# Kernel optimization log

Hardware: AMD Instinct MI355X
Metric: run time of the kernel (lower is better)

Reference implementation:

```python
import jax, jax.numpy as jnp
import numpy as np

# ogbn-products-like 3-layer GraphSAGE mini-batch: fanouts [15, 10, 5], batch 1024
N0, N1, N2, N3 = 1_000_000, 67_584, 6_144, 1_024
F_IN, HID, OUT = 100, 256, 47
FAN1, FAN2, FAN3 = 15, 10, 5
E1, E2, E3 = N1 * FAN1, N2 * FAN2, N3 * FAN3


def _glorot(key, shape):
    lim = np.sqrt(6.0 / (shape[0] + shape[1])).astype(np.float32)
    return jax.random.uniform(key, shape, jnp.float32, -lim, lim)


def setup_inputs() -> dict:
    key = jax.random.key(0)
    ks = jax.random.split(key, 12)
    x = jax.random.normal(ks[0], (N0, F_IN), jnp.float32)
    # bipartite edge lists: src indexes into the layer's source nodes,
    # dst indexes into the first n_dst nodes (the targets)
    src1 = jax.random.randint(ks[1], (E1,), 0, N0, jnp.int64)
    dst1 = jnp.repeat(jnp.arange(N1, dtype=jnp.int64), FAN1)
    src2 = jax.random.randint(ks[2], (E2,), 0, N1, jnp.int64)
    dst2 = jnp.repeat(jnp.arange(N2, dtype=jnp.int64), FAN2)
    src3 = jax.random.randint(ks[3], (E3,), 0, N2, jnp.int64)
    dst3 = jnp.repeat(jnp.arange(N3, dtype=jnp.int64), FAN3)
    return {
        "x": x,
        "W_l1": _glorot(ks[4], (F_IN, HID)), "W_r1": _glorot(ks[5], (F_IN, HID)), "b1": jnp.zeros((HID,), jnp.float32),
        "W_l2": _glorot(ks[6], (HID, HID)), "W_r2": _glorot(ks[7], (HID, HID)), "b2": jnp.zeros((HID,), jnp.float32),
        "W_l3": _glorot(ks[8], (HID, OUT)), "W_r3": _glorot(ks[9], (HID, OUT)), "b3": jnp.zeros((OUT,), jnp.float32),
        "src1": src1, "dst1": dst1, "src2": src2, "dst2": dst2, "src3": src3, "dst3": dst3,
    }


def _sage_conv(x_src, x_dst, src, dst, W_l, W_r, b, n_dst):
    # mean aggregation over incoming edges, then out = lin_l(agg) + lin_r(x_dst)
    msg = x_src[src]                                             # [E, d]
    agg = jax.ops.segment_sum(msg, dst, num_segments=n_dst)      # [n_dst, d]
    cnt = jax.ops.segment_sum(jnp.ones((src.shape[0],), x_src.dtype), dst,
                              num_segments=n_dst)
    agg = agg / jnp.maximum(cnt, 1.0)[:, None]
    return agg @ W_l + x_dst @ W_r + b


def reference(x, W_l1, W_r1, b1, W_l2, W_r2, b2, W_l3, W_r3, b3,
              src1, dst1, src2, dst2, src3, dst3):
    h = _sage_conv(x, x[:N1], src1, dst1, W_l1, W_r1, b1, N1)
    h = jax.nn.relu(h)                                           # dropout in eval mode = identity
    h = _sage_conv(h, h[:N2], src2, dst2, W_l2, W_r2, b2, N2)
    h = jax.nn.relu(h)
    h = _sage_conv(h, h[:N3], src3, dst3, W_l3, W_r3, b3, N3)
    return jax.nn.log_softmax(h, axis=-1)                        # [N3, OUT]
```

## Files before the change

### kernel.cpp

```cpp
#include <hip/hip_runtime.h>
#include <math.h>

static constexpr int cN1 = 67584, cN2 = 6144, cN3 = 1024;
static constexpr int F_IN = 100, HID = 256, OUT = 47;
static constexpr int K1P = 224;

typedef __attribute__((ext_vector_type(8))) short short8;
typedef __attribute__((ext_vector_type(4))) float float4v;

__device__ __forceinline__ ushort f2b(float f) {
    unsigned u = __builtin_bit_cast(unsigned, f);
    u += 0x7fff + ((u >> 16) & 1);
    return (ushort)(u >> 16);
}
__device__ __forceinline__ float b2f(ushort h) {
    unsigned u = ((unsigned)h) << 16;
    return __builtin_bit_cast(float, u);
}

__global__ void build_A1(const float* __restrict__ x, const int* __restrict__ src,
                         ushort* __restrict__ A1)
{
    int wave = (int)((blockIdx.x * blockDim.x + threadIdx.x) >> 6);
    int lane = threadIdx.x & 63;
    if (wave >= cN1) return;
    const int* s = src + (size_t)wave * 15;
    float ax = 0.f, ay = 0.f;
    #pragma unroll
    for (int k = 0; k < 15; ++k) {
        const float2* row = (const float2*)(x + (size_t)s[k] * F_IN);
        if (lane < 50) { float2 v = row[lane]; ax += v.x; ay += v.y; }
    }
    ushort* out = A1 + (size_t)wave * K1P;
    if (lane < 50) {
        float2 o = ((const float2*)(x + (size_t)wave * F_IN))[lane];
        ushort2 m; m.x = f2b(ax * (1.0f / 15.0f)); m.y = f2b(ay * (1.0f / 15.0f));
        ((ushort2*)out)[lane] = m;
        ushort2 d; d.x = f2b(o.x); d.y = f2b(o.y);
        *(ushort2*)(out + 100 + 2 * lane) = d;
    } else if (lane < 62) {
        ushort2 z; z.x = 0; z.y = 0;
        *(ushort2*)(out + 200 + 2 * (lane - 50)) = z;
    }
}

template<int FAN>
__global__ void build_A(const ushort* __restrict__ H, const int* __restrict__ src,
                        ushort* __restrict__ A, int M)
{
    int wave = (int)((blockIdx.x * blockDim.x + threadIdx.x) >> 6);
    int lane = threadIdx.x & 63;
    if (wave >= M) return;
    const int* s = src + (size_t)wave * FAN;
    float a0 = 0.f, a1 = 0.f, a2 = 0.f, a3 = 0.f;
    #pragma unroll
    for (int k = 0; k < FAN; ++k) {
        ushort4 v = ((const ushort4*)(H + (size_t)s[k] * HID))[lane];
        a0 += b2f(v.x); a1 += b2f(v.y); a2 += b2f(v.z); a3 += b2f(v.w);
    }
    const float inv = 1.0f / (float)FAN;
    ushort4 own = ((const ushort4*)(H + (size_t)wave * HID))[lane];
    ushort* out = A + (size_t)wave * (2 * HID);
    ushort4 m; m.x = f2b(a0 * inv); m.y = f2b(a1 * inv); m.z = f2b(a2 * inv); m.w = f2b(a3 * inv);
    ((ushort4*)out)[lane] = m;
    ((ushort4*)(out + HID))[lane] = own;
}

__global__ void conv_W(const float* __restrict__ Wl, const float* __restrict__ Wr,
                       ushort* __restrict__ Bt, int K1, int N, int Npad, int Kpad)
{
    int idx = blockIdx.x * blockDim.x + threadIdx.x;
    if (idx >= Npad * Kpad) return;
    int n = idx / Kpad, k = idx - n * Kpad;
    float v = 0.f;
    if (n < N) {
        if (k < K1)           v = Wl[(size_t)k * N + n];
        else if (k < 2 * K1)  v = Wr[(size_t)(k - K1) * N + n];
    }
    Bt[idx] = f2b(v);
}

template<bool OUT_BF16, bool RELU>
__launch_bounds__(256)
__global__ void mfma_gemm(const ushort* __restrict__ A, const ushort* __restrict__ Bt,
                          const float* __restrict__ bias, void* __restrict__ Cout,
                          int M, int N, int K)
{
    constexpr int BM = 128, BK = 32, SA = BK + 8;
    __shared__ ushort As[BM * SA];
    __shared__ ushort Bs[BM * SA];
    const int tid  = threadIdx.x;
    const int m0   = blockIdx.y * BM;
    const int n0   = blockIdx.x * BM;
    const int lane = tid & 63;
    const int w    = tid >> 6;
    const int wr   = (w >> 1) * 64;
    const int wc   = (w & 1) * 64;
    const int m_in = lane & 15;
    const int k8   = (lane >> 4) * 8;
    const int srow = tid >> 1;
    const int skc  = (tid & 1) * 16;

    float4v acc[4][4] = {};

    const ushort* gA = A  + (size_t)(m0 + srow) * K + skc;
    const ushort* gB = Bt + (size_t)(n0 + srow) * K + skc;

    for (int k0 = 0; k0 < K; k0 += BK) {
        float4 a0 = ((const float4*)(gA + k0))[0];
        float4 a1 = ((const float4*)(gA + k0))[1];
        float4 b0 = ((const float4*)(gB + k0))[0];
        float4 b1 = ((const float4*)(gB + k0))[1];
        __syncthreads();
        *(float4*)&As[srow * SA + skc]     = a0;
        *(float4*)&As[srow * SA + skc + 8] = a1;
        *(float4*)&Bs[srow * SA + skc]     = b0;
        *(float4*)&Bs[srow * SA + skc + 8] = b1;
        __syncthreads();
        short8 af[4], bf[4];
        #pragma unroll
        for (int i = 0; i < 4; ++i) {
            af[i] = *(const short8*)&As[(wr + i * 16 + m_in) * SA + k8];
            bf[i] = *(const short8*)&Bs[(wc + i * 16 + m_in) * SA + k8];
        }
        #pragma unroll
        for (int mi = 0; mi < 4; ++mi)
            #pragma unroll
            for (int ni = 0; ni < 4; ++ni)
                acc[mi][ni] = __builtin_amdgcn_mfma_f32_16x16x32_bf16(af[mi], bf[ni], acc[mi][ni], 0, 0, 0);
    }

    #pragma unroll
    for (int ni = 0; ni < 4; ++ni) {
        int col = n0 + wc + ni * 16 + m_in;
        if (col >= N) continue;
        float bv = bias[col];
        #pragma unroll
        for (int mi = 0; mi < 4; ++mi) {
            #pragma unroll
            for (int r = 0; r < 4; ++r) {
                int row = m0 + wr + mi * 16 + (lane >> 4) * 4 + r;
                float v = acc[mi][ni][r] + bv;
                if (RELU) v = fmaxf(v, 0.f);
                if (OUT_BF16) ((ushort*)Cout)[(size_t)row * N + col] = f2b(v);
                else          ((float*)Cout)[(size_t)row * N + col] = v;
            }
        }
    }
}

__global__ void logsoftmax_kernel(float* __restrict__ out, int M, int N)
{
    int wave = (int)((blockIdx.x * blockDim.x + threadIdx.x) >> 6);
    int lane = threadIdx.x & 63;
    if (wave >= M) return;
    float* row = out + (size_t)wave * N;
    float v = (lane < N) ? row[lane] : -INFINITY;
    float m = v;
    #pragma unroll
    for (int off = 32; off; off >>= 1) m = fmaxf(m, __shfl_xor(m, off));
    float e = (lane < N) ? expf(v - m) : 0.f;
    float s = e;
    #pragma unroll
    for (int off = 32; off; off >>= 1) s += __shfl_xor(s, off);
    float ls = logf(s);
    if (lane < N) row[lane] = v - m - ls;
}

extern "C" void kernel_launch(void* const* d_in, const int* in_sizes, int n_in,
                              void* d_out, int out_size, void* d_ws, size_t ws_size,
                              hipStream_t stream)
{
    const float* x    = (const float*)d_in[0];
    const float* W_l1 = (const float*)d_in[1];
    const float* W_r1 = (const float*)d_in[2];
    const float* b1   = (const float*)d_in[3];
    const float* W_l2 = (const float*)d_in[4];
    const float* W_r2 = (const float*)d_in[5];
    const float* b2   = (const float*)d_in[6];
    const float* W_l3 = (const float*)d_in[7];
    const float* W_r3 = (const float*)d_in[8];
    const float* b3   = (const float*)d_in[9];
    const int* src1 = (const int*)d_in[10];
    const int* src2 = (const int*)d_in[12];
    const int* src3 = (const int*)d_in[14];
    float* out = (float*)d_out;

    ushort* ws  = (ushort*)d_ws;
    ushort* A1  = ws;
    ushort* h1  = A1  + (size_t)cN1 * K1P;
    ushort* A2  = h1  + (size_t)cN1 * HID;
    ushort* h2  = A2  + (size_t)cN2 * 2 * HID;
    ushort* A3  = h2  + (size_t)cN2 * HID;
    ushort* Bt1 = A3  + (size_t)cN3 * 2 * HID;
    ushort* Bt2 = Bt1 + (size_t)256 * K1P;
    ushort* Bt3 = Bt2 + (size_t)256 * 2 * HID;

    conv_W<<<(256 * K1P + 255) / 256, 256, 0, stream>>>(W_l1, W_r1, Bt1, F_IN, HID, 256, K1P);
    conv_W<<<(256 * 512 + 255) / 256, 256, 0, stream>>>(W_l2, W_r2, Bt2, HID, HID, 256, 512);
    conv_W<<<(128 * 512 + 255) / 256, 256, 0, stream>>>(W_l3, W_r3, Bt3, HID, OUT, 128, 512);

    build_A1<<<cN1 / 4, 256, 0, stream>>>(x, src1, A1);
    mfma_gemm<true, true><<<dim3(2, cN1 / 128), 256, 0, stream>>>(A1, Bt1, b1, h1, cN1, HID, K1P);
    build_A<10><<<cN2 / 4, 256, 0, stream>>>(h1, src2, A2, cN2);
    mfma_gemm<true, true><<<dim3(2, cN2 / 128), 256, 0, stream>>>(A2, Bt2, b2, h2, cN2, HID, 512);
    build_A<5><<<cN3 / 4, 256, 0, stream>>>(h2, src3, A3, cN3);
    mfma_gemm<false, false><<<dim3(1, cN3 / 128), 256, 0, stream>>>(A3, Bt3, b3, out, cN3, OUT, 512);
    logsoftmax_kernel<<<cN3 / 4, 256, 0, stream>>>(out, cN3, OUT);
}
```

Measured before the change: 687.0 us.

## Widen gather loads with half-wave edge split, fuse weight conversion and log-softmax

The gather kernels now split edges between the two half-waves, which load 16-byte vectors and combine their sums with a cross-half shuffle, replacing narrower per-lane loads. The three weight-conversion launches become a single kernel, and log-softmax moves into the epilogue of the final GEMM so the last output round-trip and one launch go away. This reduces the number of memory transactions in the latency-bound gathers and the launch count. The costs are extra shuffles and more complex epilogue code.

```diff
diff --git a/kernel.cpp b/kernel.cpp
--- a/kernel.cpp
+++ b/kernel.cpp
@@ -13,9 +13,8 @@
     u += 0x7fff + ((u >> 16) & 1);
     return (ushort)(u >> 16);
 }
-__device__ __forceinline__ float b2f(ushort h) {
-    unsigned u = ((unsigned)h) << 16;
-    return __builtin_bit_cast(float, u);
+__device__ __forceinline__ unsigned pack2(float a, float b) {
+    return (unsigned)f2b(a) | ((unsigned)f2b(b) << 16);
 }
 
 __global__ void build_A1(const float* __restrict__ x, const int* __restrict__ src,
@@ -25,22 +24,40 @@
     int lane = threadIdx.x & 63;
     if (wave >= cN1) return;
     const int* s = src + (size_t)wave * 15;
-    float ax = 0.f, ay = 0.f;
-    #pragma unroll
-    for (int k = 0; k < 15; ++k) {
-        const float2* row = (const float2*)(x + (size_t)s[k] * F_IN);
-        if (lane < 50) { float2 v = row[lane]; ax += v.x; ay += v.y; }
-    }
-    ushort* out = A1 + (size_t)wave * K1P;
-    if (lane < 50) {
-        float2 o = ((const float2*)(x + (size_t)wave * F_IN))[lane];
-        ushort2 m; m.x = f2b(ax * (1.0f / 15.0f)); m.y = f2b(ay * (1.0f / 15.0f));
-        ((ushort2*)out)[lane] = m;
-        ushort2 d; d.x = f2b(o.x); d.y = f2b(o.y);
-        *(ushort2*)(out + 100 + 2 * lane) = d;
-    } else if (lane < 62) {
-        ushort2 z; z.x = 0; z.y = 0;
-        *(ushort2*)(out + 200 + 2 * (lane - 50)) = z;
+    const int half = lane >> 5, hl = lane & 31;
+    const bool act = hl < 25;
+    float4 own = {0.f, 0.f, 0.f, 0.f};
+    if (half == 1 && act)
+        own = *(const float4*)(x + (size_t)wave * F_IN + 4 * hl);
+    float4 acc = {0.f, 0.f, 0.f, 0.f};
+    #pragma unroll
+    for (int j = 0; j < 8; ++j) {
+        int e = 2 * j + half;
+        if (e < 15 && act) {
+            float4 v = *(const float4*)(x + (size_t)s[e] * F_IN + 4 * hl);
+            acc.x += v.x; acc.y += v.y; acc.z += v.z; acc.w += v.w;
+        }
+    }
+    acc.x += __shfl(acc.x, lane ^ 32);
+    acc.y += __shfl(acc.y, lane ^ 32);
+    acc.z += __shfl(acc.z, lane ^ 32);
+    acc.w += __shfl(acc.w, lane ^ 32);
+    ushort* outp = A1 + (size_t)wave * K1P;
+    constexpr float inv = 1.0f / 15.0f;
+    if (half == 0) {
+        if (act) {
+            ushort4 m; m.x = f2b(acc.x * inv); m.y = f2b(acc.y * inv);
+                       m.z = f2b(acc.z * inv); m.w = f2b(acc.w * inv);
+            *(ushort4*)(outp + 4 * hl) = m;
+        }
+    } else {
+        if (act) {
+            ushort4 d; d.x = f2b(own.x); d.y = f2b(own.y); d.z = f2b(own.z); d.w = f2b(own.w);
+            *(ushort4*)(outp + 100 + 4 * hl) = d;
+        } else if (hl < 31) {
+            ushort4 z; z.x = 0; z.y = 0; z.z = 0; z.w = 0;
+            *(ushort4*)(outp + 200 + 4 * (hl - 25)) = z;
+        }
     }
 }
 
@@ -52,35 +69,74 @@
     int lane = threadIdx.x & 63;
     if (wave >= M) return;
     const int* s = src + (size_t)wave * FAN;
-    float a0 = 0.f, a1 = 0.f, a2 = 0.f, a3 = 0.f;
-    #pragma unroll
-    for (int k = 0; k < FAN; ++k) {
-        ushort4 v = ((const ushort4*)(H + (size_t)s[k] * HID))[lane];
-        a0 += b2f(v.x); a1 += b2f(v.y); a2 += b2f(v.z); a3 += b2f(v.w);
-    }
-    const float inv = 1.0f / (float)FAN;
-    ushort4 own = ((const ushort4*)(H + (size_t)wave * HID))[lane];
-    ushort* out = A + (size_t)wave * (2 * HID);
-    ushort4 m; m.x = f2b(a0 * inv); m.y = f2b(a1 * inv); m.z = f2b(a2 * inv); m.w = f2b(a3 * inv);
-    ((ushort4*)out)[lane] = m;
-    ((ushort4*)(out + HID))[lane] = own;
-}
-
-__global__ void conv_W(const float* __restrict__ Wl, const float* __restrict__ Wr,
-                       ushort* __restrict__ Bt, int K1, int N, int Npad, int Kpad)
-{
-    int idx = blockIdx.x * blockDim.x + threadIdx.x;
-    if (idx >= Npad * Kpad) return;
-    int n = idx / Kpad, k = idx - n * Kpad;
-    float v = 0.f;
-    if (n < N) {
-        if (k < K1)           v = Wl[(size_t)k * N + n];
-        else if (k < 2 * K1)  v = Wr[(size_t)(k - K1) * N + n];
-    }
-    Bt[idx] = f2b(v);
-}
-
-template<bool OUT_BF16, bool RELU>
+    const int half = lane >> 5, hl = lane & 31;
+    const float* Hf = (const float*)H;
+    float4 own;
+    if (half == 1)
+        own = *(const float4*)(Hf + (size_t)wave * 128 + 4 * hl);
+    float a[8] = {0.f, 0.f, 0.f, 0.f, 0.f, 0.f, 0.f, 0.f};
+    constexpr int NJ = (FAN + 1) / 2;
+    #pragma unroll
+    for (int j = 0; j < NJ; ++j) {
+        int e = 2 * j + half;
+        if (e < FAN) {
+            float4 v = *(const float4*)(Hf + (size_t)s[e] * 128 + 4 * hl);
+            unsigned u;
+            u = __builtin_bit_cast(unsigned, v.x);
+            a[0] += __builtin_bit_cast(float, u << 16); a[1] += __builtin_bit_cast(float, u & 0xffff0000u);
+            u = __builtin_bit_cast(unsigned, v.y);
+            a[2] += __builtin_bit_cast(float, u << 16); a[3] += __builtin_bit_cast(float, u & 0xffff0000u);
+            u = __builtin_bit_cast(unsigned, v.z);
+            a[4] += __builtin_bit_cast(float, u << 16); a[5] += __builtin_bit_cast(float, u & 0xffff0000u);
+            u = __builtin_bit_cast(unsigned, v.w);
+            a[6] += __builtin_bit_cast(float, u << 16); a[7] += __builtin_bit_cast(float, u & 0xffff0000u);
+        }
+    }
+    #pragma unroll
+    for (int i = 0; i < 8; ++i) a[i] += __shfl(a[i], lane ^ 32);
+    ushort* outp = A + (size_t)wave * (2 * HID);
+    constexpr float inv = 1.0f / (float)FAN;
+    if (half == 0) {
+        uint4 w;
+        w.x = pack2(a[0] * inv, a[1] * inv);
+        w.y = pack2(a[2] * inv, a[3] * inv);
+        w.z = pack2(a[4] * inv, a[5] * inv);
+        w.w = pack2(a[6] * inv, a[7] * inv);
+        *(uint4*)(outp + 8 * hl) = w;
+    } else {
+        *(float4*)(outp + HID + 8 * hl) = own;
+    }
+}
+
+static constexpr int S1 = 256 * K1P, S2 = 256 * 512, S3 = 128 * 512;
+__global__ void conv_W_all(const float* __restrict__ Wl1, const float* __restrict__ Wr1,
+                           const float* __restrict__ Wl2, const float* __restrict__ Wr2,
+                           const float* __restrict__ Wl3, const float* __restrict__ Wr3,
+                           ushort* __restrict__ Bt1, ushort* __restrict__ Bt2,
+                           ushort* __restrict__ Bt3)
+{
+    int idx = blockIdx.x * 256 + threadIdx.x;
+    if (idx < S1) {
+        int n = idx / K1P, k = idx - n * K1P;
+        float v = 0.f;
+        if (k < 100)      v = Wl1[(size_t)k * 256 + n];
+        else if (k < 200) v = Wr1[(size_t)(k - 100) * 256 + n];
+        Bt1[idx] = f2b(v);
+    } else if (idx < S1 + S2) {
+        int i = idx - S1;
+        int n = i >> 9, k = i & 511;
+        float v = (k < 256) ? Wl2[(size_t)k * 256 + n] : Wr2[(size_t)(k - 256) * 256 + n];
+        Bt2[i] = f2b(v);
+    } else if (idx < S1 + S2 + S3) {
+        int i = idx - S1 - S2;
+        int n = i >> 9, k = i & 511;
+        float v = 0.f;
+        if (n < OUT) v = (k < 256) ? Wl3[(size_t)k * OUT + n] : Wr3[(size_t)(k - 256) * OUT + n];
+        Bt3[i] = f2b(v);
+    }
+}
+
+template<bool OUT_BF16, bool RELU, bool LS>
 __launch_bounds__(256)
 __global__ void mfma_gemm(const ushort* __restrict__ A, const ushort* __restrict__ Bt,
                           const float* __restrict__ bias, void* __restrict__ Cout,
@@ -130,6 +186,40 @@
                 acc[mi][ni] = __builtin_amdgcn_mfma_f32_16x16x32_bf16(af[mi], bf[ni], acc[mi][ni], 0, 0, 0);
     }
 
+    if (LS) {
+        if (wc != 0) return;
+        #pragma unroll
+        for (int mi = 0; mi < 4; ++mi) {
+            #pragma unroll
+            for (int r = 0; r < 4; ++r) {
+                float v[4]; float mx = -3.0e38f;
+                #pragma unroll
+                for (int ni = 0; ni < 4; ++ni) {
+                    int col = ni * 16 + m_in;
+                    v[ni] = (col < N) ? acc[mi][ni][r] + bias[col] : -3.0e38f;
+                    mx = fmaxf(mx, v[ni]);
+                }
+                #pragma unroll
+                for (int off = 1; off < 16; off <<= 1) mx = fmaxf(mx, __shfl_xor(mx, off));
+                float sum = 0.f;
+                #pragma unroll
+                for (int ni = 0; ni < 4; ++ni)
+                    sum += (v[ni] > -1.0e38f) ? expf(v[ni] - mx) : 0.f;
+                #pragma unroll
+                for (int off = 1; off < 16; off <<= 1) sum += __shfl_xor(sum, off);
+                float ls = logf(sum);
+                int row = m0 + wr + mi * 16 + (lane >> 4) * 4 + r;
+                #pragma unroll
+                for (int ni = 0; ni < 4; ++ni) {
+                    int col = ni * 16 + m_in;
+                    if (col < N)
+                        ((float*)Cout)[(size_t)row * N + col] = v[ni] - mx - ls;
+                }
+            }
+        }
+        return;
+    }
+
     #pragma unroll
     for (int ni = 0; ni < 4; ++ni) {
         int col = n0 + wc + ni * 16 + m_in;
@@ -147,24 +237,6 @@
             }
         }
     }
-}
-
-__global__ void logsoftmax_kernel(float* __restrict__ out, int M, int N)
-{
-    int wave = (int)((blockIdx.x * blockDim.x + threadIdx.x) >> 6);
-    int lane = threadIdx.x & 63;
-    if (wave >= M) return;
-    float* row = out + (size_t)wave * N;
-    float v = (lane < N) ? row[lane] : -INFINITY;
-    float m = v;
-    #pragma unroll
-    for (int off = 32; off; off >>= 1) m = fmaxf(m, __shfl_xor(m, off));
-    float e = (lane < N) ? expf(v - m) : 0.f;
-    float s = e;
-    #pragma unroll
-    for (int off = 32; off; off >>= 1) s += __shfl_xor(s, off);
-    float ls = logf(s);
-    if (lane < N) row[lane] = v - m - ls;
 }
 
 extern "C" void kernel_launch(void* const* d_in, const int* in_sizes, int n_in,
@@ -196,15 +268,13 @@
     ushort* Bt2 = Bt1 + (size_t)256 * K1P;
     ushort* Bt3 = Bt2 + (size_t)256 * 2 * HID;
 
-    conv_W<<<(256 * K1P + 255) / 256, 256, 0, stream>>>(W_l1, W_r1, Bt1, F_IN, HID, 256, K1P);
-    conv_W<<<(256 * 512 + 255) / 256, 256, 0, stream>>>(W_l2, W_r2, Bt2, HID, HID, 256, 512);
-    conv_W<<<(128 * 512 + 255) / 256, 256, 0, stream>>>(W_l3, W_r3, Bt3, HID, OUT, 128, 512);
+    conv_W_all<<<(S1 + S2 + S3 + 255) / 256, 256, 0, stream>>>(
+        W_l1, W_r1, W_l2, W_r2, W_l3, W_r3, Bt1, Bt2, Bt3);
 
     build_A1<<<cN1 / 4, 256, 0, stream>>>(x, src1, A1);
-    mfma_gemm<true, true><<<dim3(2, cN1 / 128), 256, 0, stream>>>(A1, Bt1, b1, h1, cN1, HID, K1P);
+    mfma_gemm<true, true, false><<<dim3(2, cN1 / 128), 256, 0, stream>>>(A1, Bt1, b1, h1, cN1, HID, K1P);
     build_A<10><<<cN2 / 4, 256, 0, stream>>>(h1, src2, A2, cN2);
-    mfma_gemm<true, true><<<dim3(2, cN2 / 128), 256, 0, stream>>>(A2, Bt2, b2, h2, cN2, HID, 512);
+    mfma_gemm<true, true, false><<<dim3(2, cN2 / 128), 256, 0, stream>>>(A2, Bt2, b2, h2, cN2, HID, 512);
     build_A<5><<<cN3 / 4, 256, 0, stream>>>(h2, src3, A3, cN3);
-    mfma_gemm<false, false><<<dim3(1, cN3 / 128), 256, 0, stream>>>(A3, Bt3, b3, out, cN3, OUT, 512);
-    logsoftmax_kernel<<<cN3 / 4, 256, 0, stream>>>(out, cN3, OUT);
-}
+    mfma_gemm<false, false, true><<<dim3(1, cN3 / 128), 256, 0, stream>>>(A3, Bt3, b3, out, cN3, OUT, 512);
+}
```

Result: faster. 654.6 us (-4.7%).
